# Kernel optimization log

Measured on AMD Instinct MI355X. Metric: run time of the kernel, lower is better.

The kernel has to match this reference:

```python
import jax, jax.numpy as jnp
import numpy as np

PIANO_SAMPLES = 2_621_440          # multiple of 256 (~119 s @ 22050 Hz)
BLOCK = 512
HOP = 256
N_STEPS = PIANO_SAMPLES // HOP      # 10240 loop iterations
N_FRAMES = PIANO_SAMPLES // HOP + 2 # 10242
UPSAMPLE = 256 // 32                # 8, as in F.upsample(scale_factor=8)


def _hamming(n=BLOCK):
    # torch.hamming_window default: periodic=True
    return (0.54 - 0.46 * jnp.cos(2.0 * jnp.pi * jnp.arange(n, dtype=jnp.float32) / n)).astype(jnp.float32)


def _upsample_linear(v, scale):
    # F.upsample(mode='linear', align_corners=False) on a 1D signal
    n = v.shape[0]
    coords = (jnp.arange(n * scale, dtype=jnp.float32) + 0.5) / scale - 0.5
    coords = jnp.clip(coords, 0.0, n - 1.0)
    lo = jnp.floor(coords).astype(jnp.int32)
    hi = jnp.minimum(lo + 1, n - 1)
    w = coords - lo.astype(jnp.float32)
    return v[lo] * (1.0 - w) + v[hi] * w


def setup_inputs() -> dict:
    key = jax.random.key(0)
    k1, k2, k3, k4, k5, k6 = jax.random.split(key, 6)
    return {
        "x": jnp.zeros((1,), jnp.float32),  # unused by the original forward
        "excitation_env": jax.random.uniform(k1, (N_FRAMES * 32,), jnp.float32) * 0.01,
        "tf_real": jax.random.uniform(k2, (N_FRAMES, 257), jnp.float32) * 0.2,
        "tf_imag": jax.random.uniform(k3, (N_FRAMES, 257), jnp.float32) * 0.2,
        "etf_real": jax.random.uniform(k4, (257,), jnp.float32) * 0.2,
        "etf_imag": jax.random.uniform(k5, (257,), jnp.float32) * 0.2,
        # per-step uniform(-1,1) noise (torch draws this inside forward)
        "noise": jax.random.uniform(k6, (N_STEPS, BLOCK), jnp.float32) * 2.0 - 1.0,
    }


def reference(x, excitation_env, tf_real, tf_imag, etf_real, etf_imag, noise):
    tf = (tf_real + 1j * tf_imag).astype(jnp.complex64)      # [N_FRAMES, 257]
    etf = (etf_real + 1j * etf_imag).astype(jnp.complex64)   # [257]
    win = _hamming()

    # excitation envelope: square then linear-upsample x8 -> len PIANO_SAMPLES + 512
    exc = _upsample_linear(excitation_env ** 2, UPSAMPLE)

    # gather all 512-sample excitation windows at hop 256 -> [N_STEPS, 512]
    idx = jnp.arange(N_STEPS)[:, None] * HOP + jnp.arange(BLOCK)[None, :]
    exc_blocks = exc[idx]

    # batched excitation filtering (independent per step -> fully vectorized)
    imp = noise * exc_blocks
    imp = jnp.fft.irfft(jnp.fft.rfft(imp, norm='ortho') * etf, norm='ortho').astype(jnp.float32)

    # impulse added to the *previous* block at steps 1..N_STEPS-1; last block gets none
    imp_next = jnp.concatenate([imp[1:], jnp.zeros((1, BLOCK), imp.dtype)], axis=0)

    def step(s, inp):
        tf_i, inext = inp
        b = win * jnp.fft.irfft(jnp.fft.rfft(s, norm='ortho') * tf_i, norm='ortho').astype(jnp.float32)
        s_next = b + inext
        return s_next, s_next

    s0 = imp[0]  # learned_impulse=False -> first block is the filtered excitation
    _, ys = jax.lax.scan(step, s0, (tf[:N_STEPS], imp_next))

    blocks = jnp.concatenate([s0[None, :], ys], axis=0)  # [N_STEPS+1, 512]

    # overlap-add with hop 256
    n_b = blocks.shape[0]
    out = jnp.zeros((n_b * HOP + (BLOCK - HOP),), blocks.dtype)
    oa_idx = jnp.arange(n_b)[:, None] * HOP + jnp.arange(BLOCK)[None, :]
    out = out.at[oa_idx].add(blocks)
    return out[:PIANO_SAMPLES]
```

## Files before the change

### kernel.cpp

```cpp
#include <hip/hip_runtime.h>
#include <math.h>

#define N_STEPS 10240
#define ROWF2 264
#define ROWF  (ROWF2*2)
#define ENV_N 327744
#define LCH 16
#define KWARM 16

typedef float f4a __attribute__((ext_vector_type(4), aligned(4)));

__device__ inline float2 mkf2(float x, float y) { return make_float2(x, y); }

template<int DIR>
__device__ inline void waveFFT256(float2 v[4], const int l,
                                  const float Tc, const float Ts,
                                  const float ux, const float uy) {
  const int rb = (int)(__brev((unsigned)l) >> 26);
  #pragma unroll
  for (int r = 0; r < 4; ++r) {
    v[r].x = __shfl(v[r].x, rb);
    v[r].y = __shfl(v[r].y, rb);
  }
  #pragma unroll
  for (int s = 0; s < 6; ++s) {
    const int half = 1 << s;
    float wx, wy;
    if (s == 0) { wx = (l & 1) ? -1.f : 1.f; wy = 0.f; }
    else {
      const int idx = (l << (5 - s)) & 63;
      wx = __shfl(Tc, idx);
      float tsv = __shfl(Ts, idx);
      wy = (DIR < 0) ? tsv : -tsv;
    }
    #pragma unroll
    for (int r = 0; r < 4; ++r) {
      float tx = __shfl_xor(v[r].x, half);
      float ty = __shfl_xor(v[r].y, half);
      const bool low = (l & half) == 0;
      float ax = low ? v[r].x : tx, ay = low ? v[r].y : ty;
      float bx = low ? tx : v[r].x, by = low ? ty : v[r].y;
      v[r].x = ax + (wx * bx - wy * by);
      v[r].y = ay + (wx * by + wy * bx);
    }
  }
  const float u2x = ux * ux - uy * uy, u2y = 2.f * ux * uy;
  const float u3x = u2x * ux - u2y * uy, u3y = u2x * uy + u2y * ux;
  float2 t0 = v[0];
  float2 t1 = mkf2(v[1].x * ux - v[1].y * uy, v[1].x * uy + v[1].y * ux);
  float2 t2 = mkf2(v[2].x * u2x - v[2].y * u2y, v[2].x * u2y + v[2].y * u2x);
  float2 t3 = mkf2(v[3].x * u3x - v[3].y * u3y, v[3].x * u3y + v[3].y * u3x);
  float2 p02 = mkf2(t0.x + t2.x, t0.y + t2.y), m02 = mkf2(t0.x - t2.x, t0.y - t2.y);
  float2 p13 = mkf2(t1.x + t3.x, t1.y + t3.y), m13 = mkf2(t1.x - t3.x, t1.y - t3.y);
  v[0] = mkf2(p02.x + p13.x, p02.y + p13.y);
  v[2] = mkf2(p02.x - p13.x, p02.y - p13.y);
  if (DIR < 0) {
    v[1] = mkf2(m02.x + m13.y, m02.y - m13.x);
    v[3] = mkf2(m02.x - m13.y, m02.y + m13.x);
  } else {
    v[1] = mkf2(m02.x - m13.y, m02.y + m13.x);
    v[3] = mkf2(m02.x + m13.y, m02.y - m13.x);
  }
}

__global__ __launch_bounds__(256) void kernA(const float* __restrict__ env,
                                             const float* __restrict__ noise,
                                             const float* __restrict__ tf_re,
                                             const float* __restrict__ etf_re,
                                             const float* __restrict__ etf_im,
                                             float* __restrict__ IMP,
                                             float* __restrict__ T256,
                                             float* __restrict__ I256) {
  const int l = threadIdx.x & 63;
  const int j = blockIdx.x * 4 + (threadIdx.x >> 6);
  float* rowf = IMP + (size_t)j * ROWF;
  float2* row = (float2*)rowf;
  if (j >= N_STEPS) {
    if (j == N_STEPS) {
      #pragma unroll
      for (int r = 0; r < 4; ++r) row[64 * r + l] = mkf2(0.f, 0.f);
      if (l == 0) { row[256] = mkf2(0.f, 0.f); I256[N_STEPS] = 0.f; }
    }
    return;
  }
  const int K = 32 * j + l;
  float e0 = env[K];                e0 *= e0;
  float em = env[max(K - 1, 0)];    em *= em;
  float ep = env[min(K + 1, ENV_N - 1)]; ep *= ep;
  float sm[8];
  #pragma unroll
  for (int u = 0; u < 8; ++u) {
    float val;
    if (u < 4) {
      float fr = 0.5625f + 0.125f * (float)u;
      val = em * (1.f - fr) + e0 * fr;
      if (K == 0) val = e0;
    } else {
      float fr = 0.0625f + 0.125f * (float)(u - 4);
      val = e0 * (1.f - fr) + ep * fr;
    }
    sm[u] = val;
  }
  const float4* np = (const float4*)(noise + (size_t)j * 512 + 8 * l);
  float4 n0 = np[0], n1 = np[1];
  float nn[8] = {n0.x, n0.y, n0.z, n0.w, n1.x, n1.y, n1.z, n1.w};
  float2 v[4];
  #pragma unroll
  for (int r = 0; r < 4; ++r)
    v[r] = mkf2(nn[2 * r] * sm[2 * r], nn[2 * r + 1] * sm[2 * r + 1]);

  float ca, sa; sincosf(-0.01227184630308513f * (float)l, &sa, &ca);
  const float ux = ca * ca - sa * sa, uy = 2.f * ca * sa;
  float Tc, Ts; sincosf(-0.09817477042468103f * (float)l, &Ts, &Tc);

  waveFFT256<-1>(v, l, Tc, Ts, ux, uy);

  float2 Zc[4];
  const int pidx = (64 - l) & 63;
  #pragma unroll
  for (int r = 0; r < 4; ++r) {
    Zc[r].x = __shfl(v[3 - r].x, pidx);
    Zc[r].y = __shfl(v[3 - r].y, pidx);
  }
  float2 z0lane = v[0];
  if (l == 0) { Zc[0] = v[0]; Zc[1] = v[3]; Zc[2] = v[2]; Zc[3] = v[1]; }
  constexpr float crA[4] = {1.f, 0.7071067811865476f, 0.f, -0.7071067811865476f};
  constexpr float srA[4] = {0.f, -0.7071067811865476f, -1.f, -0.7071067811865476f};
  const float FS = 0.04419417382415922f;
  #pragma unroll
  for (int r = 0; r < 4; ++r) {
    float Ex = 0.5f * (v[r].x + Zc[r].x), Ey = 0.5f * (v[r].y - Zc[r].y);
    float Dx = v[r].x - Zc[r].x,          Dy = v[r].y + Zc[r].y;
    float Ox = 0.5f * Dy, Oy = -0.5f * Dx;
    float c  = crA[r] * ca - srA[r] * sa;
    float sn = crA[r] * sa + srA[r] * ca;
    float Wx = (Ex + (c * Ox - sn * Oy)) * FS;
    float Wy = (Ey + (c * Oy + sn * Ox)) * FS;
    int k = 64 * r + l;
    float er = etf_re[k], ei = etf_im[k];
    float Px = Wx * er - Wy * ei;
    float Py = Wx * ei + Wy * er;
    if (k == 0) Py = 0.f;
    row[k] = mkf2(Px, Py);
  }
  if (l == 0) {
    float W256 = (z0lane.x - z0lane.y) * FS;
    float imp256 = W256 * etf_re[256];
    row[256] = mkf2(imp256, 0.f);
    I256[j] = imp256;
    T256[j] = tf_re[(size_t)j * 257 + 256];
  }
}

struct StepBuf {
  f4a tr, ti;
  float4 ia, ib;
};

__device__ inline void loadStep(StepBuf& b, int i, int l,
                                const float* __restrict__ tf_re,
                                const float* __restrict__ tf_im,
                                const float* __restrict__ IMP) {
  const size_t tb = (size_t)i * 257 + 4 * l;
  b.tr = *(const f4a*)(tf_re + tb);
  b.ti = *(const f4a*)(tf_im + tb);
  const float4* r4 = (const float4*)(IMP + (size_t)(i + 1) * ROWF);
  b.ia = r4[2 * l];
  b.ib = r4[2 * l + 1];
}

__device__ inline void doStep(int i, int j0, const StepBuf& b, int l,
                              float tfr256, float imp256,
                              float2& s0, float2& s1, float2& s2, float2& s3,
                              float& s256, float* __restrict__ S) {
  float2 y0, y1, y2, y3;
  y0.x = s0.x * b.tr[0] - s0.y * b.ti[0];  y0.y = s0.x * b.ti[0] + s0.y * b.tr[0];
  y1.x = s1.x * b.tr[1] - s1.y * b.ti[1];  y1.y = s1.x * b.ti[1] + s1.y * b.tr[1];
  y2.x = s2.x * b.tr[2] - s2.y * b.ti[2];  y2.y = s2.x * b.ti[2] + s2.y * b.tr[2];
  y3.x = s3.x * b.tr[3] - s3.y * b.ti[3];  y3.y = s3.x * b.ti[3] + s3.y * b.tr[3];
  if (l == 0) y0.y = 0.f;
  float Y256 = tfr256 * s256;
  float phx = __shfl_up(y3.x, 1), phy = __shfl_up(y3.y, 1);
  float nlx = __shfl_down(y0.x, 1), nly = __shfl_down(y0.y, 1);
  float2 p0 = (l == 0)  ? mkf2(y1.x, -y1.y) : mkf2(phx, phy);
  float2 n3 = (l == 63) ? mkf2(Y256, 0.f)   : mkf2(nlx, nly);
  float y255x = __shfl(y3.x, 63);
  const float A = 0.54f, Bc = 0.23f;
  float2 c0, c1, c2, c3;
  c0.x = A * y0.x - Bc * (p0.x + y1.x);  c0.y = A * y0.y - Bc * (p0.y + y1.y);
  c1.x = A * y1.x - Bc * (y0.x + y2.x);  c1.y = A * y1.y - Bc * (y0.y + y2.y);
  c2.x = A * y2.x - Bc * (y1.x + y3.x);  c2.y = A * y2.y - Bc * (y1.y + y3.y);
  c3.x = A * y3.x - Bc * (y2.x + n3.x);  c3.y = A * y3.y - Bc * (y2.y + n3.y);
  float C256 = A * Y256 - 0.46f * y255x;
  s0.x = c0.x + b.ia.x;  s0.y = c0.y + b.ia.y;
  s1.x = c1.x + b.ia.z;  s1.y = c1.y + b.ia.w;
  s2.x = c2.x + b.ib.x;  s2.y = c2.y + b.ib.y;
  s3.x = c3.x + b.ib.z;  s3.y = c3.y + b.ib.w;
  s256 = C256 + imp256;
  if (i >= j0) {
    float4* o4 = (float4*)(S + (size_t)(i + 1) * ROWF);
    o4[2 * l]     = make_float4(s0.x, s0.y, s1.x, s1.y);
    o4[2 * l + 1] = make_float4(s2.x, s2.y, s3.x, s3.y);
    if (l == 0) {
      S[(size_t)(i + 1) * ROWF + 512] = s256;
      S[(size_t)(i + 1) * ROWF + 513] = 0.f;
    }
  }
}

__global__ __launch_bounds__(64, 1) void kernB(const float* __restrict__ tf_re,
                                               const float* __restrict__ tf_im,
                                               const float* __restrict__ IMP,
                                               const float* __restrict__ T256,
                                               const float* __restrict__ I256,
                                               float* __restrict__ S) {
  const int c = blockIdx.x, l = threadIdx.x;
  const int j0 = c * LCH;
  const int jend = min(j0 + LCH, N_STEPS);
  const int w0 = max(0, j0 - KWARM);
  const int last = jend - 1;
  const float t256v = T256[min(w0 + l, N_STEPS - 1)];
  const float i256v = I256[min(w0 + 1 + l, N_STEPS)];
  float2 s0 = mkf2(0.f, 0.f), s1 = s0, s2 = s0, s3 = s0;
  float s256 = 0.f;
  if (c == 0) {
    const float4* r4 = (const float4*)IMP;
    float4 a = r4[2 * l], bb = r4[2 * l + 1];
    s0 = mkf2(a.x, a.y);  s1 = mkf2(a.z, a.w);
    s2 = mkf2(bb.x, bb.y); s3 = mkf2(bb.z, bb.w);
    s256 = IMP[512];
    float4* o4 = (float4*)S;
    o4[2 * l] = a; o4[2 * l + 1] = bb;
    if (l == 0) { S[512] = s256; S[513] = 0.f; }
  }
  StepBuf b0, b1, b2, b3, b4, b5, b6, b7;
  loadStep(b0, w0 + 0, l, tf_re, tf_im, IMP);
  loadStep(b1, w0 + 1, l, tf_re, tf_im, IMP);
  loadStep(b2, w0 + 2, l, tf_re, tf_im, IMP);
  loadStep(b3, w0 + 3, l, tf_re, tf_im, IMP);
  loadStep(b4, w0 + 4, l, tf_re, tf_im, IMP);
  loadStep(b5, w0 + 5, l, tf_re, tf_im, IMP);
  loadStep(b6, w0 + 6, l, tf_re, tf_im, IMP);
  loadStep(b7, w0 + 7, l, tf_re, tf_im, IMP);
  int i = w0;
  #define STEP8(BUF) { \
    const int m = i - w0; \
    const float tfr_ = __shfl(t256v, m); \
    const float im2_ = __shfl(i256v, m); \
    doStep(i, j0, BUF, l, tfr_, im2_, s0, s1, s2, s3, s256, S); \
    int nx = i + 8; nx = (nx > last) ? last : nx; \
    loadStep(BUF, nx, l, tf_re, tf_im, IMP); \
    ++i; }
  while (i < jend) {
    STEP8(b0) STEP8(b1) STEP8(b2) STEP8(b3)
    STEP8(b4) STEP8(b5) STEP8(b6) STEP8(b7)
  }
  #undef STEP8
}

__global__ __launch_bounds__(576) void kernC(const float* __restrict__ S,
                                             float* __restrict__ out) {
  const int l = threadIdx.x & 63;
  const int w = threadIdx.x >> 6;
  const int b = blockIdx.x;
  const int r = 8 * b - 1 + w;
  __shared__ float2 ybuf[9][256];
  if (r < 0) {
    #pragma unroll
    for (int rr = 0; rr < 4; ++rr) ybuf[0][64 * rr + l] = mkf2(0.f, 0.f);
  } else {
    const float2* row = (const float2*)(S + (size_t)r * ROWF);
    const float4* r4 = (const float4*)row;
    float4 a = r4[2 * l], bb = r4[2 * l + 1];
    float2 W[4] = {mkf2(a.x, a.y), mkf2(a.z, a.w), mkf2(bb.x, bb.y), mkf2(bb.z, bb.w)};
    float w256 = row[256].x;
    float2 Wm[4];
    const int pidx = (64 - l) & 63;
    Wm[0].x = __shfl(W[0].x, pidx);
    Wm[0].y = __shfl(W[0].y, pidx);
    if (l == 0) Wm[0] = mkf2(w256, 0.f);
    Wm[1].x = __shfl_xor(W[3].x, 63);  Wm[1].y = __shfl_xor(W[3].y, 63);
    Wm[2].x = __shfl_xor(W[2].x, 63);  Wm[2].y = __shfl_xor(W[2].y, 63);
    Wm[3].x = __shfl_xor(W[1].x, 63);  Wm[3].y = __shfl_xor(W[1].y, 63);
    float cu, su; sincosf(0.02454369260617026f * (float)l, &su, &cu);
    const float cl = cu * cu - su * su, sl_ = 2.f * cu * su;
    float Tc, Ts; sincosf(-0.09817477042468103f * (float)l, &Ts, &Tc);
    constexpr float crC[4] = {1.f, 0.9999247018391445f, 0.9996988186962042f, 0.9993223845883495f};
    constexpr float srC[4] = {0.f, 0.0122715382857199f, 0.0245412285229123f, 0.0368072229413588f};
    float2 v[4];
    #pragma unroll
    for (int rr = 0; rr < 4; ++rr) {
      float Ex = 0.5f * (W[rr].x + Wm[rr].x), Ey = 0.5f * (W[rr].y - Wm[rr].y);
      float Dx = W[rr].x - Wm[rr].x,          Dy = W[rr].y + Wm[rr].y;
      float c  = cl * crC[rr] - sl_ * srC[rr];
      float sn = cl * srC[rr] + sl_ * crC[rr];
      float Ox = 0.5f * (c * Dx - sn * Dy);
      float Oy = 0.5f * (c * Dy + sn * Dx);
      v[rr] = mkf2(Ex - Oy, Ey + Ox);
    }
    waveFFT256<+1>(v, l, Tc, Ts, cu, su);
    const float ISC = 0.08838834764831845f;
    #pragma unroll
    for (int rr = 0; rr < 4; ++rr)
      ybuf[w][64 * rr + l] = mkf2(v[rr].x * ISC, v[rr].y * ISC);
  }
  __syncthreads();
  float2* out2 = (float2*)out;
  const size_t base = (size_t)b * 1024;
  for (int idx = threadIdx.x; idx < 1024; idx += 576) {
    const int k = idx >> 7, t2 = idx & 127;
    float2 a = ybuf[k + 1][t2];
    float2 p = ybuf[k][128 + t2];
    out2[base + idx] = mkf2(a.x + p.x, a.y + p.y);
  }
}

extern "C" void kernel_launch(void* const* d_in, const int* in_sizes, int n_in,
                              void* d_out, int out_size, void* d_ws, size_t ws_size,
                              hipStream_t stream) {
  const float* env    = (const float*)d_in[1];
  const float* tf_re  = (const float*)d_in[2];
  const float* tf_im  = (const float*)d_in[3];
  const float* etf_re = (const float*)d_in[4];
  const float* etf_im = (const float*)d_in[5];
  const float* noise  = (const float*)d_in[6];
  float* out = (float*)d_out;

  float* wsf = (float*)d_ws;
  float* IMP  = wsf;
  float* S    = wsf + (size_t)(N_STEPS + 1) * ROWF;
  float* T256 = wsf + (size_t)2 * (N_STEPS + 1) * ROWF;
  float* I256 = T256 + N_STEPS;

  kernA<<<(N_STEPS / 4) + 1, 256, 0, stream>>>(env, noise, tf_re, etf_re, etf_im,
                                               IMP, T256, I256);
  kernB<<<N_STEPS / LCH, 64, 0, stream>>>(tf_re, tf_im, IMP, T256, I256, S);
  kernC<<<N_STEPS / 8, 576, 0, stream>>>(S, out);
}
```

Measured before the change: 54.22 us.

## Fuse scan and inverse-FFT overlap-add into one kernel with inline-asm prefetch

Merges the chunked recurrence kernel with the inverse real FFT and overlap-add stage. Each block now inverse-transforms its states in registers and writes output samples directly, carrying the tail half across steps, so the intermediate spectrum buffer S and a third launch go away. Step-data prefetch now uses inline-asm global loads with explicit vmcnt waits and sched barriers to keep eight slots in flight. The cost is an added 256-point wave FFT on the serial per-step critical path of a kernel that runs one wave per block, and fragile hand-managed wait counts.

```diff
diff --git a/kernel.cpp b/kernel.cpp
--- a/kernel.cpp
+++ b/kernel.cpp
@@ -8,7 +8,7 @@
 #define LCH 16
 #define KWARM 16
 
-typedef float f4a __attribute__((ext_vector_type(4), aligned(4)));
+typedef float f4 __attribute__((ext_vector_type(4)));
 
 __device__ inline float2 mkf2(float x, float y) { return make_float2(x, y); }
 
@@ -152,27 +152,24 @@
   }
 }
 
-struct StepBuf {
-  f4a tr, ti;
-  float4 ia, ib;
-};
-
-__device__ inline void loadStep(StepBuf& b, int i, int l,
-                                const float* __restrict__ tf_re,
-                                const float* __restrict__ tf_im,
-                                const float* __restrict__ IMP) {
-  const size_t tb = (size_t)i * 257 + 4 * l;
-  b.tr = *(const f4a*)(tf_re + tb);
-  b.ti = *(const f4a*)(tf_im + tb);
-  const float4* r4 = (const float4*)(IMP + (size_t)(i + 1) * ROWF);
-  b.ia = r4[2 * l];
-  b.ib = r4[2 * l + 1];
-}
-
-__device__ inline void doStep(int i, int j0, const StepBuf& b, int l,
-                              float tfr256, float imp256,
+struct Slot { f4 tr, ti, ia, ib; };
+
+__device__ inline void issueSlot(Slot& b, int i, int l,
+                                 const float* __restrict__ tf_re,
+                                 const float* __restrict__ tf_im,
+                                 const float* __restrict__ IMP) {
+  const float* atr = tf_re + (size_t)i * 257 + 4 * l;
+  const float* ati = tf_im + (size_t)i * 257 + 4 * l;
+  const float* aim = IMP + (size_t)(i + 1) * ROWF + 8 * l;
+  asm volatile("global_load_dwordx4 %0, %1, off" : "=v"(b.tr) : "v"(atr));
+  asm volatile("global_load_dwordx4 %0, %1, off" : "=v"(b.ti) : "v"(ati));
+  asm volatile("global_load_dwordx4 %0, %1, off" : "=v"(b.ia) : "v"(aim));
+  asm volatile("global_load_dwordx4 %0, %1, off offset:16" : "=v"(b.ib) : "v"(aim));
+}
+
+__device__ inline void doStep(const Slot& b, int l, float tfr256, float imp256,
                               float2& s0, float2& s1, float2& s2, float2& s3,
-                              float& s256, float* __restrict__ S) {
+                              float& s256) {
   float2 y0, y1, y2, y3;
   y0.x = s0.x * b.tr[0] - s0.y * b.ti[0];  y0.y = s0.x * b.ti[0] + s0.y * b.tr[0];
   y1.x = s1.x * b.tr[1] - s1.y * b.ti[1];  y1.y = s1.x * b.ti[1] + s1.y * b.tr[1];
@@ -192,127 +189,123 @@
   c2.x = A * y2.x - Bc * (y1.x + y3.x);  c2.y = A * y2.y - Bc * (y1.y + y3.y);
   c3.x = A * y3.x - Bc * (y2.x + n3.x);  c3.y = A * y3.y - Bc * (y2.y + n3.y);
   float C256 = A * Y256 - 0.46f * y255x;
-  s0.x = c0.x + b.ia.x;  s0.y = c0.y + b.ia.y;
-  s1.x = c1.x + b.ia.z;  s1.y = c1.y + b.ia.w;
-  s2.x = c2.x + b.ib.x;  s2.y = c2.y + b.ib.y;
-  s3.x = c3.x + b.ib.z;  s3.y = c3.y + b.ib.w;
+  s0.x = c0.x + b.ia[0];  s0.y = c0.y + b.ia[1];
+  s1.x = c1.x + b.ia[2];  s1.y = c1.y + b.ia[3];
+  s2.x = c2.x + b.ib[0];  s2.y = c2.y + b.ib[1];
+  s3.x = c3.x + b.ib[2];  s3.y = c3.y + b.ib[3];
   s256 = C256 + imp256;
-  if (i >= j0) {
-    float4* o4 = (float4*)(S + (size_t)(i + 1) * ROWF);
-    o4[2 * l]     = make_float4(s0.x, s0.y, s1.x, s1.y);
-    o4[2 * l + 1] = make_float4(s2.x, s2.y, s3.x, s3.y);
-    if (l == 0) {
-      S[(size_t)(i + 1) * ROWF + 512] = s256;
-      S[(size_t)(i + 1) * ROWF + 513] = 0.f;
-    }
-  }
-}
-
-__global__ __launch_bounds__(64, 1) void kernB(const float* __restrict__ tf_re,
-                                               const float* __restrict__ tf_im,
-                                               const float* __restrict__ IMP,
-                                               const float* __restrict__ T256,
-                                               const float* __restrict__ I256,
-                                               float* __restrict__ S) {
+}
+
+__device__ inline void ifftState(float2 v[4],
+                                 float2 s0, float2 s1, float2 s2, float2 s3,
+                                 float s256, int l,
+                                 float clC, float slC, float Tc, float Ts,
+                                 float cu, float su) {
+  float2 W[4] = {s0, s1, s2, s3};
+  float2 Wm[4];
+  const int pidx = (64 - l) & 63;
+  Wm[0].x = __shfl(W[0].x, pidx);
+  Wm[0].y = __shfl(W[0].y, pidx);
+  if (l == 0) Wm[0] = mkf2(s256, 0.f);
+  Wm[1].x = __shfl_xor(W[3].x, 63);  Wm[1].y = __shfl_xor(W[3].y, 63);
+  Wm[2].x = __shfl_xor(W[2].x, 63);  Wm[2].y = __shfl_xor(W[2].y, 63);
+  Wm[3].x = __shfl_xor(W[1].x, 63);  Wm[3].y = __shfl_xor(W[1].y, 63);
+  constexpr float crC[4] = {1.f, 0.9999247018391445f, 0.9996988186962042f, 0.9993223845883495f};
+  constexpr float srC[4] = {0.f, 0.0122715382857199f, 0.0245412285229123f, 0.0368072229413588f};
+  #pragma unroll
+  for (int rr = 0; rr < 4; ++rr) {
+    float Ex = 0.5f * (W[rr].x + Wm[rr].x), Ey = 0.5f * (W[rr].y - Wm[rr].y);
+    float Dx = W[rr].x - Wm[rr].x,          Dy = W[rr].y + Wm[rr].y;
+    float c  = clC * crC[rr] - slC * srC[rr];
+    float sn = clC * srC[rr] + slC * crC[rr];
+    float Ox = 0.5f * (c * Dx - sn * Dy);
+    float Oy = 0.5f * (c * Dy + sn * Dx);
+    v[rr] = mkf2(Ex - Oy, Ey + Ox);
+  }
+  waveFFT256<+1>(v, l, Tc, Ts, cu, su);
+}
+
+__global__ __launch_bounds__(64, 1) void kernBC(const float* __restrict__ tf_re,
+                                                const float* __restrict__ tf_im,
+                                                const float* __restrict__ IMP,
+                                                const float* __restrict__ T256,
+                                                const float* __restrict__ I256,
+                                                float* __restrict__ out) {
   const int c = blockIdx.x, l = threadIdx.x;
   const int j0 = c * LCH;
-  const int jend = min(j0 + LCH, N_STEPS);
+  const int jend = j0 + LCH;
   const int w0 = max(0, j0 - KWARM);
   const int last = jend - 1;
-  const float t256v = T256[min(w0 + l, N_STEPS - 1)];
-  const float i256v = I256[min(w0 + 1 + l, N_STEPS)];
+  float2* out2 = (float2*)out;
+  const float ISC = 0.08838834764831845f;
+
+  float t256v = T256[min(w0 + l, N_STEPS - 1)];
+  float i256v = I256[min(w0 + 1 + l, N_STEPS)];
+
+  float cu, su; sincosf(0.02454369260617026f * (float)l, &su, &cu);
+  const float clC = cu * cu - su * su, slC = 2.f * cu * su;
+  float Tc, Ts; sincosf(-0.09817477042468103f * (float)l, &Ts, &Tc);
+
   float2 s0 = mkf2(0.f, 0.f), s1 = s0, s2 = s0, s3 = s0;
   float s256 = 0.f;
+  float2 pt0 = mkf2(0.f, 0.f), pt1 = pt0;
+
   if (c == 0) {
     const float4* r4 = (const float4*)IMP;
     float4 a = r4[2 * l], bb = r4[2 * l + 1];
     s0 = mkf2(a.x, a.y);  s1 = mkf2(a.z, a.w);
     s2 = mkf2(bb.x, bb.y); s3 = mkf2(bb.z, bb.w);
     s256 = IMP[512];
-    float4* o4 = (float4*)S;
-    o4[2 * l] = a; o4[2 * l + 1] = bb;
-    if (l == 0) { S[512] = s256; S[513] = 0.f; }
-  }
-  StepBuf b0, b1, b2, b3, b4, b5, b6, b7;
-  loadStep(b0, w0 + 0, l, tf_re, tf_im, IMP);
-  loadStep(b1, w0 + 1, l, tf_re, tf_im, IMP);
-  loadStep(b2, w0 + 2, l, tf_re, tf_im, IMP);
-  loadStep(b3, w0 + 3, l, tf_re, tf_im, IMP);
-  loadStep(b4, w0 + 4, l, tf_re, tf_im, IMP);
-  loadStep(b5, w0 + 5, l, tf_re, tf_im, IMP);
-  loadStep(b6, w0 + 6, l, tf_re, tf_im, IMP);
-  loadStep(b7, w0 + 7, l, tf_re, tf_im, IMP);
+    float2 v[4];
+    ifftState(v, s0, s1, s2, s3, s256, l, clC, slC, Tc, Ts, cu, su);
+    out2[l]      = mkf2(v[0].x * ISC, v[0].y * ISC);
+    out2[64 + l] = mkf2(v[1].x * ISC, v[1].y * ISC);
+    pt0 = mkf2(v[2].x * ISC, v[2].y * ISC);
+    pt1 = mkf2(v[3].x * ISC, v[3].y * ISC);
+  }
+
+  asm volatile("" :: "v"(t256v), "v"(i256v));
+  asm volatile("s_waitcnt vmcnt(0)" ::: "memory");
+
+  Slot b0, b1, b2, b3, b4, b5, b6, b7;
+  issueSlot(b0, w0 + 0, l, tf_re, tf_im, IMP);
+  issueSlot(b1, w0 + 1, l, tf_re, tf_im, IMP);
+  issueSlot(b2, w0 + 2, l, tf_re, tf_im, IMP);
+  issueSlot(b3, w0 + 3, l, tf_re, tf_im, IMP);
+  issueSlot(b4, w0 + 4, l, tf_re, tf_im, IMP);
+  issueSlot(b5, w0 + 5, l, tf_re, tf_im, IMP);
+  issueSlot(b6, w0 + 6, l, tf_re, tf_im, IMP);
+  issueSlot(b7, w0 + 7, l, tf_re, tf_im, IMP);
+
+  const int rlo   = (c == 0) ? 1 : (j0 - 1);
+  const int remit = (c == 0) ? 1 : j0;
   int i = w0;
   #define STEP8(BUF) { \
+    asm volatile("s_waitcnt vmcnt(28)" ::: "memory"); \
+    __builtin_amdgcn_sched_barrier(0); \
     const int m = i - w0; \
     const float tfr_ = __shfl(t256v, m); \
     const float im2_ = __shfl(i256v, m); \
-    doStep(i, j0, BUF, l, tfr_, im2_, s0, s1, s2, s3, s256, S); \
+    doStep(BUF, l, tfr_, im2_, s0, s1, s2, s3, s256); \
+    const int r = i + 1; \
+    if (r >= rlo && r < jend) { \
+      float2 v[4]; \
+      ifftState(v, s0, s1, s2, s3, s256, l, clC, slC, Tc, Ts, cu, su); \
+      if (r >= remit) { \
+        out2[(size_t)r * 128 + l]      = mkf2(v[0].x * ISC + pt0.x, v[0].y * ISC + pt0.y); \
+        out2[(size_t)r * 128 + 64 + l] = mkf2(v[1].x * ISC + pt1.x, v[1].y * ISC + pt1.y); \
+      } \
+      pt0 = mkf2(v[2].x * ISC, v[2].y * ISC); \
+      pt1 = mkf2(v[3].x * ISC, v[3].y * ISC); \
+    } \
     int nx = i + 8; nx = (nx > last) ? last : nx; \
-    loadStep(BUF, nx, l, tf_re, tf_im, IMP); \
+    issueSlot(BUF, nx, l, tf_re, tf_im, IMP); \
     ++i; }
   while (i < jend) {
     STEP8(b0) STEP8(b1) STEP8(b2) STEP8(b3)
     STEP8(b4) STEP8(b5) STEP8(b6) STEP8(b7)
   }
   #undef STEP8
-}
-
-__global__ __launch_bounds__(576) void kernC(const float* __restrict__ S,
-                                             float* __restrict__ out) {
-  const int l = threadIdx.x & 63;
-  const int w = threadIdx.x >> 6;
-  const int b = blockIdx.x;
-  const int r = 8 * b - 1 + w;
-  __shared__ float2 ybuf[9][256];
-  if (r < 0) {
-    #pragma unroll
-    for (int rr = 0; rr < 4; ++rr) ybuf[0][64 * rr + l] = mkf2(0.f, 0.f);
-  } else {
-    const float2* row = (const float2*)(S + (size_t)r * ROWF);
-    const float4* r4 = (const float4*)row;
-    float4 a = r4[2 * l], bb = r4[2 * l + 1];
-    float2 W[4] = {mkf2(a.x, a.y), mkf2(a.z, a.w), mkf2(bb.x, bb.y), mkf2(bb.z, bb.w)};
-    float w256 = row[256].x;
-    float2 Wm[4];
-    const int pidx = (64 - l) & 63;
-    Wm[0].x = __shfl(W[0].x, pidx);
-    Wm[0].y = __shfl(W[0].y, pidx);
-    if (l == 0) Wm[0] = mkf2(w256, 0.f);
-    Wm[1].x = __shfl_xor(W[3].x, 63);  Wm[1].y = __shfl_xor(W[3].y, 63);
-    Wm[2].x = __shfl_xor(W[2].x, 63);  Wm[2].y = __shfl_xor(W[2].y, 63);
-    Wm[3].x = __shfl_xor(W[1].x, 63);  Wm[3].y = __shfl_xor(W[1].y, 63);
-    float cu, su; sincosf(0.02454369260617026f * (float)l, &su, &cu);
-    const float cl = cu * cu - su * su, sl_ = 2.f * cu * su;
-    float Tc, Ts; sincosf(-0.09817477042468103f * (float)l, &Ts, &Tc);
-    constexpr float crC[4] = {1.f, 0.9999247018391445f, 0.9996988186962042f, 0.9993223845883495f};
-    constexpr float srC[4] = {0.f, 0.0122715382857199f, 0.0245412285229123f, 0.0368072229413588f};
-    float2 v[4];
-    #pragma unroll
-    for (int rr = 0; rr < 4; ++rr) {
-      float Ex = 0.5f * (W[rr].x + Wm[rr].x), Ey = 0.5f * (W[rr].y - Wm[rr].y);
-      float Dx = W[rr].x - Wm[rr].x,          Dy = W[rr].y + Wm[rr].y;
-      float c  = cl * crC[rr] - sl_ * srC[rr];
-      float sn = cl * srC[rr] + sl_ * crC[rr];
-      float Ox = 0.5f * (c * Dx - sn * Dy);
-      float Oy = 0.5f * (c * Dy + sn * Dx);
-      v[rr] = mkf2(Ex - Oy, Ey + Ox);
-    }
-    waveFFT256<+1>(v, l, Tc, Ts, cu, su);
-    const float ISC = 0.08838834764831845f;
-    #pragma unroll
-    for (int rr = 0; rr < 4; ++rr)
-      ybuf[w][64 * rr + l] = mkf2(v[rr].x * ISC, v[rr].y * ISC);
-  }
-  __syncthreads();
-  float2* out2 = (float2*)out;
-  const size_t base = (size_t)b * 1024;
-  for (int idx = threadIdx.x; idx < 1024; idx += 576) {
-    const int k = idx >> 7, t2 = idx & 127;
-    float2 a = ybuf[k + 1][t2];
-    float2 p = ybuf[k][128 + t2];
-    out2[base + idx] = mkf2(a.x + p.x, a.y + p.y);
-  }
 }
 
 extern "C" void kernel_launch(void* const* d_in, const int* in_sizes, int n_in,
@@ -328,12 +321,10 @@
 
   float* wsf = (float*)d_ws;
   float* IMP  = wsf;
-  float* S    = wsf + (size_t)(N_STEPS + 1) * ROWF;
-  float* T256 = wsf + (size_t)2 * (N_STEPS + 1) * ROWF;
+  float* T256 = wsf + (size_t)(N_STEPS + 1) * ROWF;
   float* I256 = T256 + N_STEPS;
 
   kernA<<<(N_STEPS / 4) + 1, 256, 0, stream>>>(env, noise, tf_re, etf_re, etf_im,
                                                IMP, T256, I256);
-  kernB<<<N_STEPS / LCH, 64, 0, stream>>>(tf_re, tf_im, IMP, T256, I256, S);
-  kernC<<<N_STEPS / 8, 576, 0, stream>>>(S, out);
-}
+  kernBC<<<N_STEPS / LCH, 64, 0, stream>>>(tf_re, tf_im, IMP, T256, I256, out);
+}
```

Result: slower. 58.81 us (+8.5%).

## Spread kernB recurrence across 256 threads, one frequency bin each

Applied to the files above, without the earlier changes.

The per-chunk recurrence kernel changes from one 64-lane wavefront, where each lane handles four bins, to a 256-thread block where each thread owns a single bin. Neighbour bins for the Hamming convolution come from wave shuffles, and wave-boundary values are exchanged through double-buffered shared memory with a __syncthreads each step. This shortens each thread's serial work and its register footprint, at the price of a block-wide barrier in every step of the dependent chain. Loads become scalar per bin instead of float4.

```diff
diff --git a/kernel.cpp b/kernel.cpp
--- a/kernel.cpp
+++ b/kernel.cpp
@@ -152,110 +152,100 @@
   }
 }
 
-struct StepBuf {
-  f4a tr, ti;
-  float4 ia, ib;
-};
-
-__device__ inline void loadStep(StepBuf& b, int i, int l,
+struct StepBuf { float tr, ti; float2 im; };
+
+__device__ inline void loadStep(StepBuf& b, int i, int bin,
                                 const float* __restrict__ tf_re,
                                 const float* __restrict__ tf_im,
                                 const float* __restrict__ IMP) {
-  const size_t tb = (size_t)i * 257 + 4 * l;
-  b.tr = *(const f4a*)(tf_re + tb);
-  b.ti = *(const f4a*)(tf_im + tb);
-  const float4* r4 = (const float4*)(IMP + (size_t)(i + 1) * ROWF);
-  b.ia = r4[2 * l];
-  b.ib = r4[2 * l + 1];
-}
-
-__device__ inline void doStep(int i, int j0, const StepBuf& b, int l,
-                              float tfr256, float imp256,
-                              float2& s0, float2& s1, float2& s2, float2& s3,
-                              float& s256, float* __restrict__ S) {
-  float2 y0, y1, y2, y3;
-  y0.x = s0.x * b.tr[0] - s0.y * b.ti[0];  y0.y = s0.x * b.ti[0] + s0.y * b.tr[0];
-  y1.x = s1.x * b.tr[1] - s1.y * b.ti[1];  y1.y = s1.x * b.ti[1] + s1.y * b.tr[1];
-  y2.x = s2.x * b.tr[2] - s2.y * b.ti[2];  y2.y = s2.x * b.ti[2] + s2.y * b.tr[2];
-  y3.x = s3.x * b.tr[3] - s3.y * b.ti[3];  y3.y = s3.x * b.ti[3] + s3.y * b.tr[3];
-  if (l == 0) y0.y = 0.f;
-  float Y256 = tfr256 * s256;
-  float phx = __shfl_up(y3.x, 1), phy = __shfl_up(y3.y, 1);
-  float nlx = __shfl_down(y0.x, 1), nly = __shfl_down(y0.y, 1);
-  float2 p0 = (l == 0)  ? mkf2(y1.x, -y1.y) : mkf2(phx, phy);
-  float2 n3 = (l == 63) ? mkf2(Y256, 0.f)   : mkf2(nlx, nly);
-  float y255x = __shfl(y3.x, 63);
-  const float A = 0.54f, Bc = 0.23f;
-  float2 c0, c1, c2, c3;
-  c0.x = A * y0.x - Bc * (p0.x + y1.x);  c0.y = A * y0.y - Bc * (p0.y + y1.y);
-  c1.x = A * y1.x - Bc * (y0.x + y2.x);  c1.y = A * y1.y - Bc * (y0.y + y2.y);
-  c2.x = A * y2.x - Bc * (y1.x + y3.x);  c2.y = A * y2.y - Bc * (y1.y + y3.y);
-  c3.x = A * y3.x - Bc * (y2.x + n3.x);  c3.y = A * y3.y - Bc * (y2.y + n3.y);
-  float C256 = A * Y256 - 0.46f * y255x;
-  s0.x = c0.x + b.ia.x;  s0.y = c0.y + b.ia.y;
-  s1.x = c1.x + b.ia.z;  s1.y = c1.y + b.ia.w;
-  s2.x = c2.x + b.ib.x;  s2.y = c2.y + b.ib.y;
-  s3.x = c3.x + b.ib.z;  s3.y = c3.y + b.ib.w;
-  s256 = C256 + imp256;
-  if (i >= j0) {
-    float4* o4 = (float4*)(S + (size_t)(i + 1) * ROWF);
-    o4[2 * l]     = make_float4(s0.x, s0.y, s1.x, s1.y);
-    o4[2 * l + 1] = make_float4(s2.x, s2.y, s3.x, s3.y);
-    if (l == 0) {
-      S[(size_t)(i + 1) * ROWF + 512] = s256;
-      S[(size_t)(i + 1) * ROWF + 513] = 0.f;
-    }
-  }
-}
-
-__global__ __launch_bounds__(64, 1) void kernB(const float* __restrict__ tf_re,
-                                               const float* __restrict__ tf_im,
-                                               const float* __restrict__ IMP,
-                                               const float* __restrict__ T256,
-                                               const float* __restrict__ I256,
-                                               float* __restrict__ S) {
-  const int c = blockIdx.x, l = threadIdx.x;
+  b.tr = tf_re[(size_t)i * 257 + bin];
+  b.ti = tf_im[(size_t)i * 257 + bin];
+  b.im = ((const float2*)(IMP + (size_t)(i + 1) * ROWF))[bin];
+}
+
+__global__ __launch_bounds__(256, 1) void kernB(const float* __restrict__ tf_re,
+                                                const float* __restrict__ tf_im,
+                                                const float* __restrict__ IMP,
+                                                const float* __restrict__ T256,
+                                                const float* __restrict__ I256,
+                                                float* __restrict__ S) {
+  const int c = blockIdx.x;
+  const int tid = threadIdx.x;
+  const int lane = tid & 63;
+  const int w = tid >> 6;
+  const int bin = tid;
+  const bool nyq = (tid == 255);
   const int j0 = c * LCH;
-  const int jend = min(j0 + LCH, N_STEPS);
-  const int w0 = max(0, j0 - KWARM);
+  const int jend = j0 + LCH;
+  const int w0 = (c > 0) ? (j0 - KWARM) : 0;
   const int last = jend - 1;
-  const float t256v = T256[min(w0 + l, N_STEPS - 1)];
-  const float i256v = I256[min(w0 + 1 + l, N_STEPS)];
-  float2 s0 = mkf2(0.f, 0.f), s1 = s0, s2 = s0, s3 = s0;
+
+  __shared__ float2 edge[2][4][2];
+
+  const float t256v = T256[min(w0 + lane, N_STEPS - 1)];
+  const float i256v = I256[min(w0 + 1 + lane, N_STEPS)];
+
+  float2 sb = mkf2(0.f, 0.f);
   float s256 = 0.f;
+
   if (c == 0) {
-    const float4* r4 = (const float4*)IMP;
-    float4 a = r4[2 * l], bb = r4[2 * l + 1];
-    s0 = mkf2(a.x, a.y);  s1 = mkf2(a.z, a.w);
-    s2 = mkf2(bb.x, bb.y); s3 = mkf2(bb.z, bb.w);
-    s256 = IMP[512];
-    float4* o4 = (float4*)S;
-    o4[2 * l] = a; o4[2 * l + 1] = bb;
-    if (l == 0) { S[512] = s256; S[513] = 0.f; }
-  }
+    sb = ((const float2*)IMP)[bin];
+    ((float2*)S)[bin] = sb;
+    if (nyq) { s256 = IMP[512]; S[512] = s256; S[513] = 0.f; }
+  }
+
   StepBuf b0, b1, b2, b3, b4, b5, b6, b7;
-  loadStep(b0, w0 + 0, l, tf_re, tf_im, IMP);
-  loadStep(b1, w0 + 1, l, tf_re, tf_im, IMP);
-  loadStep(b2, w0 + 2, l, tf_re, tf_im, IMP);
-  loadStep(b3, w0 + 3, l, tf_re, tf_im, IMP);
-  loadStep(b4, w0 + 4, l, tf_re, tf_im, IMP);
-  loadStep(b5, w0 + 5, l, tf_re, tf_im, IMP);
-  loadStep(b6, w0 + 6, l, tf_re, tf_im, IMP);
-  loadStep(b7, w0 + 7, l, tf_re, tf_im, IMP);
+  loadStep(b0, w0 + 0, bin, tf_re, tf_im, IMP);
+  loadStep(b1, w0 + 1, bin, tf_re, tf_im, IMP);
+  loadStep(b2, w0 + 2, bin, tf_re, tf_im, IMP);
+  loadStep(b3, w0 + 3, bin, tf_re, tf_im, IMP);
+  loadStep(b4, w0 + 4, bin, tf_re, tf_im, IMP);
+  loadStep(b5, w0 + 5, bin, tf_re, tf_im, IMP);
+  loadStep(b6, w0 + 6, bin, tf_re, tf_im, IMP);
+  loadStep(b7, w0 + 7, bin, tf_re, tf_im, IMP);
+
   int i = w0;
-  #define STEP8(BUF) { \
+  #define STEP(BUF) { \
     const int m = i - w0; \
-    const float tfr_ = __shfl(t256v, m); \
+    const float tfr_ = __shfl(t256v, m);      \
     const float im2_ = __shfl(i256v, m); \
-    doStep(i, j0, BUF, l, tfr_, im2_, s0, s1, s2, s3, s256, S); \
-    int nx = i + 8; nx = (nx > last) ? last : nx; \
-    loadStep(BUF, nx, l, tf_re, tf_im, IMP); \
+    float2 y; \
+    y.x = sb.x * BUF.tr - sb.y * BUF.ti; \
+    y.y = sb.x * BUF.ti + sb.y * BUF.tr; \
+    if (bin == 0) y.y = 0.f;                  \
+    const float Y256 = tfr_ * s256;           \
+    const int p = i & 1; \
+    if (lane == 0)  edge[p][w][0] = y; \
+    if (lane == 63) edge[p][w][1] = y; \
+    __syncthreads(); \
+    float2 yp, ym; \
+    yp.x = __shfl_down(y.x, 1);  yp.y = __shfl_down(y.y, 1); \
+    ym.x = __shfl_up(y.x, 1);    ym.y = __shfl_up(y.y, 1); \
+    if (lane == 63 && w < 3) yp = edge[p][w + 1][0]; \
+    if (lane == 0  && w > 0) ym = edge[p][w - 1][1]; \
+    if (bin == 0) ym = mkf2(yp.x, -yp.y);     \
+    if (nyq)      yp = mkf2(Y256, 0.f);       \
+    float2 cc; \
+    cc.x = 0.54f * y.x - 0.23f * (ym.x + yp.x); \
+    cc.y = 0.54f * y.y - 0.23f * (ym.y + yp.y); \
+    sb.x = cc.x + BUF.im.x; \
+    sb.y = cc.y + BUF.im.y; \
+    if (nyq) s256 = 0.54f * Y256 - 0.46f * y.x + im2_;   \
+    if (i >= j0) { \
+      ((float2*)(S + (size_t)(i + 1) * ROWF))[bin] = sb; \
+      if (nyq) { \
+        S[(size_t)(i + 1) * ROWF + 512] = s256; \
+        S[(size_t)(i + 1) * ROWF + 513] = 0.f; \
+      } \
+    } \
+    { int nx = i + 8; nx = (nx > last) ? last : nx; loadStep(BUF, nx, bin, tf_re, tf_im, IMP); } \
     ++i; }
+
   while (i < jend) {
-    STEP8(b0) STEP8(b1) STEP8(b2) STEP8(b3)
-    STEP8(b4) STEP8(b5) STEP8(b6) STEP8(b7)
-  }
-  #undef STEP8
+    STEP(b0) STEP(b1) STEP(b2) STEP(b3)
+    STEP(b4) STEP(b5) STEP(b6) STEP(b7)
+  }
+  #undef STEP
 }
 
 __global__ __launch_bounds__(576) void kernC(const float* __restrict__ S,
@@ -334,6 +324,6 @@
 
   kernA<<<(N_STEPS / 4) + 1, 256, 0, stream>>>(env, noise, tf_re, etf_re, etf_im,
                                                IMP, T256, I256);
-  kernB<<<N_STEPS / LCH, 64, 0, stream>>>(tf_re, tf_im, IMP, T256, I256, S);
+  kernB<<<N_STEPS / LCH, 256, 0, stream>>>(tf_re, tf_im, IMP, T256, I256, S);
   kernC<<<N_STEPS / 8, 576, 0, stream>>>(S, out);
 }
```

Measured after the change: 57.50 us. +6.1%, slower.

## Fuse recurrence and inverse-FFT overlap-add kernels, keeping spectra in registers

Applied to the files above, without the earlier changes.

Merges the chunked spectral recurrence kernel and the inverse-FFT/overlap-add kernel into one 256-thread block per 16-step chunk. All four waves run the recurrence redundantly, and each keeps a quarter of the resulting spectra in registers, so the intermediate S buffer no longer makes a global round trip. The warm-up length drops from 16 steps to 9 and the prefetch depth from 8 to 4. This removes a kernel launch and global traffic but quadruples the recurrence work per chunk, and the shorter warm-up may hurt accuracy.

```diff
diff --git a/kernel.cpp b/kernel.cpp
--- a/kernel.cpp
+++ b/kernel.cpp
@@ -6,7 +6,6 @@
 #define ROWF  (ROWF2*2)
 #define ENV_N 327744
 #define LCH 16
-#define KWARM 16
 
 typedef float f4a __attribute__((ext_vector_type(4), aligned(4)));
 
@@ -152,10 +151,7 @@
   }
 }
 
-struct StepBuf {
-  f4a tr, ti;
-  float4 ia, ib;
-};
+struct StepBuf { f4a tr, ti; float4 ia, ib; };
 
 __device__ inline void loadStep(StepBuf& b, int i, int l,
                                 const float* __restrict__ tf_re,
@@ -169,10 +165,9 @@
   b.ib = r4[2 * l + 1];
 }
 
-__device__ inline void doStep(int i, int j0, const StepBuf& b, int l,
-                              float tfr256, float imp256,
+__device__ inline void doStep(const StepBuf& b, int l, float tfr256, float imp256,
                               float2& s0, float2& s1, float2& s2, float2& s3,
-                              float& s256, float* __restrict__ S) {
+                              float& s256) {
   float2 y0, y1, y2, y3;
   y0.x = s0.x * b.tr[0] - s0.y * b.ti[0];  y0.y = s0.x * b.ti[0] + s0.y * b.tr[0];
   y1.x = s1.x * b.tr[1] - s1.y * b.ti[1];  y1.y = s1.x * b.ti[1] + s1.y * b.tr[1];
@@ -197,117 +192,124 @@
   s2.x = c2.x + b.ib.x;  s2.y = c2.y + b.ib.y;
   s3.x = c3.x + b.ib.z;  s3.y = c3.y + b.ib.w;
   s256 = C256 + imp256;
-  if (i >= j0) {
-    float4* o4 = (float4*)(S + (size_t)(i + 1) * ROWF);
-    o4[2 * l]     = make_float4(s0.x, s0.y, s1.x, s1.y);
-    o4[2 * l + 1] = make_float4(s2.x, s2.y, s3.x, s3.y);
-    if (l == 0) {
-      S[(size_t)(i + 1) * ROWF + 512] = s256;
-      S[(size_t)(i + 1) * ROWF + 513] = 0.f;
-    }
-  }
-}
-
-__global__ __launch_bounds__(64, 1) void kernB(const float* __restrict__ tf_re,
-                                               const float* __restrict__ tf_im,
-                                               const float* __restrict__ IMP,
-                                               const float* __restrict__ T256,
-                                               const float* __restrict__ I256,
-                                               float* __restrict__ S) {
-  const int c = blockIdx.x, l = threadIdx.x;
+}
+
+__global__ __launch_bounds__(256, 2) void kernBC(const float* __restrict__ tf_re,
+                                                 const float* __restrict__ tf_im,
+                                                 const float* __restrict__ IMP,
+                                                 const float* __restrict__ T256,
+                                                 const float* __restrict__ I256,
+                                                 float* __restrict__ out) {
+  const int c = blockIdx.x, tid = threadIdx.x;
+  const int l = tid & 63, w = tid >> 6;
   const int j0 = c * LCH;
-  const int jend = min(j0 + LCH, N_STEPS);
-  const int w0 = max(0, j0 - KWARM);
-  const int last = jend - 1;
-  const float t256v = T256[min(w0 + l, N_STEPS - 1)];
-  const float i256v = I256[min(w0 + 1 + l, N_STEPS)];
+  const int w0 = (c > 0) ? (j0 - 9) : 0;
+  const int lastStep = (c > 0) ? (j0 + 14) : 15;
+
+  __shared__ float2 ybuf[17][256];
+
+  float t256v = T256[min(w0 + l, N_STEPS - 1)];
+  float i256v = I256[min(w0 + 1 + l, N_STEPS)];
+
   float2 s0 = mkf2(0.f, 0.f), s1 = s0, s2 = s0, s3 = s0;
   float s256 = 0.f;
+  float2 rs[5][4];
+  float rn[5];
+  #pragma unroll
+  for (int q = 0; q < 5; ++q) {
+    rs[q][0] = rs[q][1] = rs[q][2] = rs[q][3] = mkf2(0.f, 0.f);
+    rn[q] = 0.f;
+  }
+
   if (c == 0) {
     const float4* r4 = (const float4*)IMP;
     float4 a = r4[2 * l], bb = r4[2 * l + 1];
     s0 = mkf2(a.x, a.y);  s1 = mkf2(a.z, a.w);
     s2 = mkf2(bb.x, bb.y); s3 = mkf2(bb.z, bb.w);
     s256 = IMP[512];
-    float4* o4 = (float4*)S;
-    o4[2 * l] = a; o4[2 * l + 1] = bb;
-    if (l == 0) { S[512] = s256; S[513] = 0.f; }
-  }
-  StepBuf b0, b1, b2, b3, b4, b5, b6, b7;
+    if (w == 1) { rs[0][0]=s0; rs[0][1]=s1; rs[0][2]=s2; rs[0][3]=s3; rn[0]=s256; }
+  }
+
+  StepBuf b0, b1, b2, b3;
   loadStep(b0, w0 + 0, l, tf_re, tf_im, IMP);
   loadStep(b1, w0 + 1, l, tf_re, tf_im, IMP);
   loadStep(b2, w0 + 2, l, tf_re, tf_im, IMP);
   loadStep(b3, w0 + 3, l, tf_re, tf_im, IMP);
-  loadStep(b4, w0 + 4, l, tf_re, tf_im, IMP);
-  loadStep(b5, w0 + 5, l, tf_re, tf_im, IMP);
-  loadStep(b6, w0 + 6, l, tf_re, tf_im, IMP);
-  loadStep(b7, w0 + 7, l, tf_re, tf_im, IMP);
-  int i = w0;
-  #define STEP8(BUF) { \
-    const int m = i - w0; \
-    const float tfr_ = __shfl(t256v, m); \
-    const float im2_ = __shfl(i256v, m); \
-    doStep(i, j0, BUF, l, tfr_, im2_, s0, s1, s2, s3, s256, S); \
-    int nx = i + 8; nx = (nx > last) ? last : nx; \
-    loadStep(BUF, nx, l, tf_re, tf_im, IMP); \
-    ++i; }
-  while (i < jend) {
-    STEP8(b0) STEP8(b1) STEP8(b2) STEP8(b3)
-    STEP8(b4) STEP8(b5) STEP8(b6) STEP8(b7)
-  }
-  #undef STEP8
-}
-
-__global__ __launch_bounds__(576) void kernC(const float* __restrict__ S,
-                                             float* __restrict__ out) {
-  const int l = threadIdx.x & 63;
-  const int w = threadIdx.x >> 6;
-  const int b = blockIdx.x;
-  const int r = 8 * b - 1 + w;
-  __shared__ float2 ybuf[9][256];
-  if (r < 0) {
-    #pragma unroll
-    for (int rr = 0; rr < 4; ++rr) ybuf[0][64 * rr + l] = mkf2(0.f, 0.f);
+
+  #define SAVEIF(KK) \
+    if ((KK) >= 0 && (KK) <= 16 && (((KK) & 3) == w)) { \
+      const int _q = (((KK) > 0 ? (KK) : 0)) >> 2; \
+      rs[_q][0]=s0; rs[_q][1]=s1; rs[_q][2]=s2; rs[_q][3]=s3; rn[_q]=s256; }
+
+  #define STEP(BUF, M, KK) { \
+    const float tfr_ = __shfl(t256v, (M)); \
+    const float im2_ = __shfl(i256v, (M)); \
+    doStep(BUF, l, tfr_, im2_, s0, s1, s2, s3, s256); \
+    SAVEIF(KK) \
+    { int nx = w0 + (M) + 4; nx = (nx > lastStep) ? lastStep : nx; \
+      loadStep(BUF, nx, l, tf_re, tf_im, IMP); } }
+
+  if (c > 0) {
+    STEP(b0,0,-7)  STEP(b1,1,-6)  STEP(b2,2,-5)  STEP(b3,3,-4)
+    STEP(b0,4,-3)  STEP(b1,5,-2)  STEP(b2,6,-1)  STEP(b3,7,0)
+    STEP(b0,8,1)   STEP(b1,9,2)   STEP(b2,10,3)  STEP(b3,11,4)
+    STEP(b0,12,5)  STEP(b1,13,6)  STEP(b2,14,7)  STEP(b3,15,8)
+    STEP(b0,16,9)  STEP(b1,17,10) STEP(b2,18,11) STEP(b3,19,12)
+    STEP(b0,20,13) STEP(b1,21,14) STEP(b2,22,15) STEP(b3,23,16)
   } else {
-    const float2* row = (const float2*)(S + (size_t)r * ROWF);
-    const float4* r4 = (const float4*)row;
-    float4 a = r4[2 * l], bb = r4[2 * l + 1];
-    float2 W[4] = {mkf2(a.x, a.y), mkf2(a.z, a.w), mkf2(bb.x, bb.y), mkf2(bb.z, bb.w)};
-    float w256 = row[256].x;
-    float2 Wm[4];
-    const int pidx = (64 - l) & 63;
-    Wm[0].x = __shfl(W[0].x, pidx);
-    Wm[0].y = __shfl(W[0].y, pidx);
-    if (l == 0) Wm[0] = mkf2(w256, 0.f);
-    Wm[1].x = __shfl_xor(W[3].x, 63);  Wm[1].y = __shfl_xor(W[3].y, 63);
-    Wm[2].x = __shfl_xor(W[2].x, 63);  Wm[2].y = __shfl_xor(W[2].y, 63);
-    Wm[3].x = __shfl_xor(W[1].x, 63);  Wm[3].y = __shfl_xor(W[1].y, 63);
-    float cu, su; sincosf(0.02454369260617026f * (float)l, &su, &cu);
-    const float cl = cu * cu - su * su, sl_ = 2.f * cu * su;
-    float Tc, Ts; sincosf(-0.09817477042468103f * (float)l, &Ts, &Tc);
-    constexpr float crC[4] = {1.f, 0.9999247018391445f, 0.9996988186962042f, 0.9993223845883495f};
-    constexpr float srC[4] = {0.f, 0.0122715382857199f, 0.0245412285229123f, 0.0368072229413588f};
-    float2 v[4];
-    #pragma unroll
-    for (int rr = 0; rr < 4; ++rr) {
-      float Ex = 0.5f * (W[rr].x + Wm[rr].x), Ey = 0.5f * (W[rr].y - Wm[rr].y);
-      float Dx = W[rr].x - Wm[rr].x,          Dy = W[rr].y + Wm[rr].y;
-      float c  = cl * crC[rr] - sl_ * srC[rr];
-      float sn = cl * srC[rr] + sl_ * crC[rr];
-      float Ox = 0.5f * (c * Dx - sn * Dy);
-      float Oy = 0.5f * (c * Dy + sn * Dx);
-      v[rr] = mkf2(Ex - Oy, Ey + Ox);
-    }
-    waveFFT256<+1>(v, l, Tc, Ts, cu, su);
-    const float ISC = 0.08838834764831845f;
-    #pragma unroll
-    for (int rr = 0; rr < 4; ++rr)
-      ybuf[w][64 * rr + l] = mkf2(v[rr].x * ISC, v[rr].y * ISC);
-  }
+    STEP(b0,0,2)   STEP(b1,1,3)   STEP(b2,2,4)   STEP(b3,3,5)
+    STEP(b0,4,6)   STEP(b1,5,7)   STEP(b2,6,8)   STEP(b3,7,9)
+    STEP(b0,8,10)  STEP(b1,9,11)  STEP(b2,10,12) STEP(b3,11,13)
+    STEP(b0,12,14) STEP(b1,13,15) STEP(b2,14,16) STEP(b3,15,17)
+  }
+  #undef STEP
+  #undef SAVEIF
+
+  float cu, su; sincosf(0.02454369260617026f * (float)l, &su, &cu);
+  const float clC = cu * cu - su * su, slC = 2.f * cu * su;
+  float Tc, Ts; sincosf(-0.09817477042468103f * (float)l, &Ts, &Tc);
+  constexpr float crC[4] = {1.f, 0.9999247018391445f, 0.9996988186962042f, 0.9993223845883495f};
+  constexpr float srC[4] = {0.f, 0.0122715382857199f, 0.0245412285229123f, 0.0368072229413588f};
+  const float ISC = 0.08838834764831845f;
+  const int pidx = (64 - l) & 63;
+
+  #pragma unroll
+  for (int q = 0; q < 5; ++q) {
+    const int k = 4 * q + w;
+    if (k <= 16) {
+      float2 W0 = rs[q][0], W1 = rs[q][1], W2 = rs[q][2], W3 = rs[q][3];
+      float w256 = rn[q];
+      float2 W[4] = {W0, W1, W2, W3};
+      float2 Wm[4];
+      Wm[0].x = __shfl(W0.x, pidx);
+      Wm[0].y = __shfl(W0.y, pidx);
+      if (l == 0) Wm[0] = mkf2(w256, 0.f);
+      Wm[1].x = __shfl_xor(W3.x, 63);  Wm[1].y = __shfl_xor(W3.y, 63);
+      Wm[2].x = __shfl_xor(W2.x, 63);  Wm[2].y = __shfl_xor(W2.y, 63);
+      Wm[3].x = __shfl_xor(W1.x, 63);  Wm[3].y = __shfl_xor(W1.y, 63);
+      float2 v[4];
+      #pragma unroll
+      for (int rr = 0; rr < 4; ++rr) {
+        float Ex = 0.5f * (W[rr].x + Wm[rr].x), Ey = 0.5f * (W[rr].y - Wm[rr].y);
+        float Dx = W[rr].x - Wm[rr].x,          Dy = W[rr].y + Wm[rr].y;
+        float cc  = clC * crC[rr] - slC * srC[rr];
+        float sn  = clC * srC[rr] + slC * crC[rr];
+        float Ox = 0.5f * (cc * Dx - sn * Dy);
+        float Oy = 0.5f * (cc * Dy + sn * Dx);
+        v[rr] = mkf2(Ex - Oy, Ey + Ox);
+      }
+      waveFFT256<+1>(v, l, Tc, Ts, cu, su);
+      #pragma unroll
+      for (int rr = 0; rr < 4; ++rr)
+        ybuf[k][64 * rr + l] = mkf2(v[rr].x * ISC, v[rr].y * ISC);
+    }
+  }
+
   __syncthreads();
+
   float2* out2 = (float2*)out;
-  const size_t base = (size_t)b * 1024;
-  for (int idx = threadIdx.x; idx < 1024; idx += 576) {
+  const size_t base = (size_t)j0 * 128;
+  for (int idx = tid; idx < 2048; idx += 256) {
     const int k = idx >> 7, t2 = idx & 127;
     float2 a = ybuf[k + 1][t2];
     float2 p = ybuf[k][128 + t2];
@@ -328,12 +330,10 @@
 
   float* wsf = (float*)d_ws;
   float* IMP  = wsf;
-  float* S    = wsf + (size_t)(N_STEPS + 1) * ROWF;
-  float* T256 = wsf + (size_t)2 * (N_STEPS + 1) * ROWF;
+  float* T256 = wsf + (size_t)(N_STEPS + 1) * ROWF;
   float* I256 = T256 + N_STEPS;
 
   kernA<<<(N_STEPS / 4) + 1, 256, 0, stream>>>(env, noise, tf_re, etf_re, etf_im,
                                                IMP, T256, I256);
-  kernB<<<N_STEPS / LCH, 64, 0, stream>>>(tf_re, tf_im, IMP, T256, I256, S);
-  kernC<<<N_STEPS / 8, 576, 0, stream>>>(S, out);
-}
+  kernBC<<<N_STEPS / LCH, 256, 0, stream>>>(tf_re, tf_im, IMP, T256, I256, out);
+}
```

Result: faster. 49.73 us, median of 2 (-8.3%).
